# Performance work log

Measured on AMD Instinct MI355X. Metric: run time of the kernel, lower is better.

Reference implementation:

```python
import jax, jax.numpy as jnp
import numpy as np

N, DIN, C, E = 50000, 256, 8, 1600000
N_STEPS = 5


def setup_inputs() -> dict:
    key = jax.random.key(0)
    k1, k2, k3, k4 = jax.random.split(key, 4)
    x = jax.random.normal(k1, (N, DIN), dtype=jnp.float32)
    W = jax.random.normal(k2, (DIN, C), dtype=jnp.float32) / np.float32(np.sqrt(DIN))
    b = jnp.zeros((C,), dtype=jnp.float32)
    edge_index = jax.random.randint(k3, (2, E), 0, N, dtype=jnp.int64)
    rv = jax.random.randint(k4, (E,), 0, E, dtype=jnp.int64)
    return {"x": x, "W": W, "b": b, "edge_index": edge_index, "rv": rv}


def _log_normalize(lx):
    return lx - jax.scipy.special.logsumexp(lx, axis=-1, keepdims=True)


def reference(x, W, b, edge_index, rv):
    # transform: Linear (num_hidden=0) + LogSoftmax -> initial log beliefs
    log_b0 = jax.nn.log_softmax(x @ W + b, axis=-1)            # [N, C]
    src, dst = edge_index[0], edge_index[1]
    n_nodes, n_cls = log_b0.shape
    # learn_coupling=False: log_H = -3 * (ones - eye)
    logH = -3.0 * (jnp.ones((n_cls, n_cls), jnp.float32) - jnp.eye(n_cls, dtype=jnp.float32))
    log_msg = jnp.full((edge_index.shape[1], n_cls), -np.log(n_cls), dtype=jnp.float32)
    log_b = log_b0
    for _ in range(N_STEPS):
        x_j = log_b[src]                                        # [E, C] gather
        t = x_j - log_msg[rv]                                   # [E, C]
        # per-edge logsumexp over incoming class dim against coupling matrix
        raw = jax.scipy.special.logsumexp(t[:, :, None] + logH[None, :, :], axis=1)  # [E, C]
        log_msg = _log_normalize(raw)
        agg = jax.ops.segment_sum(log_msg, dst, num_segments=n_nodes)  # scatter-add
        log_b = _log_normalize(agg + log_b0)
    return log_b
```

## Files before the change

### kernel.cpp

```cpp
#include <hip/hip_runtime.h>

static constexpr int kN   = 50000;
static constexpr int kDin = 256;
static constexpr int kC   = 8;
static constexpr int kE   = 1600000;
static constexpr int kSteps = 5;

static constexpr int kNB      = 256;
static constexpr int kBucketW = 196;
static constexpr int kChunk   = 4096;
static constexpr int kEperB   = kE / kNB;

static constexpr size_t OFF_LOGB0 = 0;
static constexpr size_t OFF_BHIST = 1600000;
static constexpr size_t OFF_GBASE = 1601024;
static constexpr size_t OFF_GCUR  = 1602112;
static constexpr size_t OFF_START = 1603200;
static constexpr size_t OFF_REC   = 1803264;
static constexpr size_t OFF_INV   = 8203264;
static constexpr size_t OFF_MSGA  = 14603264;
static constexpr size_t OFF_MSGB  = 40203264;
static constexpr size_t OFF_SPOS  = 65803264;
static constexpr size_t OFF_SRCS  = 72203264;
static constexpr size_t OFF_RVS   = 78603264;
static constexpr size_t OFF_REC2  = 85003264;
static constexpr size_t OFF_GCUR2 = 97803264;
static constexpr size_t WS_NEEDED = 97804288;

static constexpr float kDEC   = 3.0f / 65535.0f;
static constexpr float kENC   = 65535.0f / 3.0f;
static constexpr float kOFF   = 3.2990003f;
static constexpr float kA     = 0.049787068367863944f;
static constexpr float kOneMA = 0.950212931632136f;

__global__ void __launch_bounds__(256) init_kernel(
    const float* __restrict__ x, const float* __restrict__ W,
    const float* __restrict__ bias,
    float* __restrict__ log_b0, float* __restrict__ log_b,
    const int* __restrict__ dst, int* __restrict__ bhist)
{
    __shared__ int h[kNB];
    if (blockIdx.x >= 1024) {
        h[threadIdx.x] = 0;
        __syncthreads();
        const int nthr = 256 * 256;
        for (int e = (blockIdx.x - 1024) * 256 + threadIdx.x; e < kE; e += nthr)
            atomicAdd(&h[dst[e] / kBucketW], 1);
        __syncthreads();
        if (h[threadIdx.x]) atomicAdd(&bhist[threadIdx.x], h[threadIdx.x]);
        return;
    }

    const int lane   = threadIdx.x & 63;
    const int wave   = (blockIdx.x * 256 + threadIdx.x) >> 6;
    const int nwaves = (1024 * 256) >> 6;

    float w[4][8];
#pragma unroll
    for (int j = 0; j < 4; ++j) {
        const float4* wp = reinterpret_cast<const float4*>(W + (size_t)(lane + 64 * j) * kC);
        float4 a = wp[0], b2 = wp[1];
        w[j][0] = a.x;  w[j][1] = a.y;  w[j][2] = a.z;  w[j][3] = a.w;
        w[j][4] = b2.x; w[j][5] = b2.y; w[j][6] = b2.z; w[j][7] = b2.w;
    }

    for (int row = wave; row < kN; row += nwaves) {
        const float* xr = x + (size_t)row * kDin;
        float acc[8] = {0.f, 0.f, 0.f, 0.f, 0.f, 0.f, 0.f, 0.f};
#pragma unroll
        for (int j = 0; j < 4; ++j) {
            float xv = xr[lane + 64 * j];
#pragma unroll
            for (int c = 0; c < 8; ++c) acc[c] = fmaf(xv, w[j][c], acc[c]);
        }
#pragma unroll
        for (int off = 32; off > 0; off >>= 1) {
#pragma unroll
            for (int c = 0; c < 8; ++c) acc[c] += __shfl_down(acc[c], off, 64);
        }
        if (lane == 0) {
            float z[8], m = -1e30f;
#pragma unroll
            for (int c = 0; c < 8; ++c) { z[c] = acc[c] + bias[c]; m = fmaxf(m, z[c]); }
            float s = 0.f;
#pragma unroll
            for (int c = 0; c < 8; ++c) s += __expf(z[c] - m);
            float lse = m + __logf(s);
#pragma unroll
            for (int c = 0; c < 8; ++c) {
                float v = z[c] - lse;
                log_b0[(size_t)row * 8 + c] = v;
                log_b[(size_t)row * 8 + c]  = v;
            }
        }
    }
}

__global__ void __launch_bounds__(256) bucket_scan_kernel(
    const int* __restrict__ bhist, int* __restrict__ gbase, int* __restrict__ gcur,
    int* __restrict__ gcur2)
{
    __shared__ int sh[kNB];
    const int tid = threadIdx.x;
    int v = bhist[tid];
    sh[tid] = v;
    __syncthreads();
#pragma unroll
    for (int off = 1; off < kNB; off <<= 1) {
        int t = (tid >= off) ? sh[tid - off] : 0;
        __syncthreads();
        sh[tid] += t;
        __syncthreads();
    }
    int excl = sh[tid] - v;
    gbase[tid] = excl;
    gcur[tid]  = excl;
    gcur2[tid] = tid * kEperB;
    if (tid == kNB - 1) { gbase[kNB] = sh[tid]; gcur[kNB] = sh[tid]; }
}

__global__ void __launch_bounds__(256) bin_kernel(
    const int* __restrict__ dst, int* __restrict__ gcur,
    unsigned int* __restrict__ recbuf)
{
    __shared__ int hist[kNB];
    __shared__ int sh[kNB];
    __shared__ int cursor[kNB];
    __shared__ int gdbase[kNB];
    __shared__ unsigned int buf[kChunk];

    const int tid = threadIdx.x;
    const int e0  = blockIdx.x * kChunk;
    const int n   = (kE - e0 < kChunk) ? (kE - e0) : kChunk;

    hist[tid] = 0;
    __syncthreads();

    int myb[16];
    unsigned int rec[16];
#pragma unroll
    for (int k = 0; k < 16; ++k) {
        const int i = tid + k * 256;
        myb[k] = -1;
        if (i < n) {
            const int d = dst[e0 + i];
            const int b = d / kBucketW;
            myb[k] = b;
            rec[k] = ((unsigned int)(d - b * kBucketW) << 21) | (unsigned int)(e0 + i);
            atomicAdd(&hist[b], 1);
        }
    }
    __syncthreads();

    const int cnt = hist[tid];
    sh[tid] = cnt;
    __syncthreads();
#pragma unroll
    for (int off = 1; off < kNB; off <<= 1) {
        int t = (tid >= off) ? sh[tid - off] : 0;
        __syncthreads();
        sh[tid] += t;
        __syncthreads();
    }
    const int excl = sh[tid] - cnt;
    cursor[tid] = excl;
    __syncthreads();

#pragma unroll
    for (int k = 0; k < 16; ++k) {
        if (myb[k] >= 0) {
            int slot = atomicAdd(&cursor[myb[k]], 1);
            buf[slot] = rec[k];
        }
    }
    gdbase[tid] = (cnt > 0) ? atomicAdd(&gcur[tid], cnt) : 0;
    __syncthreads();

    for (int i = tid; i < n; i += 256) {
        int b = 0;
#pragma unroll
        for (int step = 128; step >= 1; step >>= 1)
            if (b + step <= kNB - 1 && sh[b + step - 1] <= i) b += step;
        const int off_in_b = i - (sh[b] - hist[b]);
        recbuf[gdbase[b] + off_in_b] = buf[i];
    }
}

__global__ void __launch_bounds__(256) fine_kernel(
    const int* __restrict__ gbase, const unsigned int* __restrict__ recbuf,
    int* __restrict__ start, int* __restrict__ inv)
{
    __shared__ int hist[kNB];
    __shared__ int sh[kNB];
    __shared__ int lcur[kNB];

    const int tid = threadIdx.x;
    const int b   = blockIdx.x;
    const int nb0 = b * kBucketW;
    const int nnode = (kN - nb0 < kBucketW) ? (kN - nb0) : kBucketW;
    const int rb = gbase[b], re = gbase[b + 1];

    hist[tid] = 0;
    __syncthreads();

    for (int i = rb + tid; i < re; i += 256)
        atomicAdd(&hist[recbuf[i] >> 21], 1);
    __syncthreads();

    const int cnt = hist[tid];
    sh[tid] = cnt;
    __syncthreads();
#pragma unroll
    for (int off = 1; off < kNB; off <<= 1) {
        int t = (tid >= off) ? sh[tid - off] : 0;
        __syncthreads();
        sh[tid] += t;
        __syncthreads();
    }
    const int excl = sh[tid] - cnt;
    lcur[tid] = rb + excl;
    if (tid < nnode) start[nb0 + tid] = rb + excl;
    if (b == gridDim.x - 1 && tid == 0) start[kN] = kE;
    __syncthreads();

    for (int i = rb + tid; i < re; i += 256) {
        const unsigned int r = recbuf[i];
        const int p = atomicAdd(&lcur[r >> 21], 1);
        inv[p] = (int)(r & 0x1FFFFFu);
    }
}

__global__ void __launch_bounds__(256) bin2_kernel(
    const int* __restrict__ inv, int* __restrict__ gcur2,
    unsigned long long* __restrict__ recbuf2)
{
    __shared__ int hist[kNB];
    __shared__ int sh[kNB];
    __shared__ int cursor[kNB];
    __shared__ int gdbase[kNB];
    __shared__ unsigned long long buf[kChunk];

    const int tid = threadIdx.x;
    const int p0  = blockIdx.x * kChunk;
    const int n   = (kE - p0 < kChunk) ? (kE - p0) : kChunk;

    hist[tid] = 0;
    __syncthreads();

    int myb[16];
    unsigned long long rec[16];
#pragma unroll
    for (int k = 0; k < 16; ++k) {
        const int i = tid + k * 256;
        myb[k] = -1;
        if (i < n) {
            const int e = inv[p0 + i];
            const int b = e / kEperB;
            myb[k] = b;
            rec[k] = ((unsigned long long)(e - b * kEperB) << 32) | (unsigned int)(p0 + i);
            atomicAdd(&hist[b], 1);
        }
    }
    __syncthreads();

    const int cnt = hist[tid];
    sh[tid] = cnt;
    __syncthreads();
#pragma unroll
    for (int off = 1; off < kNB; off <<= 1) {
        int t = (tid >= off) ? sh[tid - off] : 0;
        __syncthreads();
        sh[tid] += t;
        __syncthreads();
    }
    const int excl = sh[tid] - cnt;
    cursor[tid] = excl;
    __syncthreads();

#pragma unroll
    for (int k = 0; k < 16; ++k) {
        if (myb[k] >= 0) {
            int slot = atomicAdd(&cursor[myb[k]], 1);
            buf[slot] = rec[k];
        }
    }
    gdbase[tid] = (cnt > 0) ? atomicAdd(&gcur2[tid], cnt) : 0;
    __syncthreads();

    for (int i = tid; i < n; i += 256) {
        int b = 0;
#pragma unroll
        for (int step = 128; step >= 1; step >>= 1)
            if (b + step <= kNB - 1 && sh[b + step - 1] <= i) b += step;
        const int off_in_b = i - (sh[b] - hist[b]);
        recbuf2[gdbase[b] + off_in_b] = buf[i];
    }
}

__global__ void __launch_bounds__(256) fine2_kernel(
    const unsigned long long* __restrict__ recbuf2, int* __restrict__ spos)
{
    __shared__ int slot[kEperB];
    const int tid  = threadIdx.x;
    const int base = blockIdx.x * kEperB;

    for (int i = tid; i < kEperB; i += 256) {
        const unsigned long long r = recbuf2[base + i];
        slot[(int)(r >> 32)] = (int)(r & 0xFFFFFFFFu);
    }
    __syncthreads();
    for (int i = tid; i < kEperB; i += 256)
        spos[base + i] = slot[i];
}

__global__ void __launch_bounds__(256) build_kernel(
    const int* __restrict__ inv, const int* __restrict__ src,
    const int* __restrict__ rv, const int* __restrict__ spos,
    int* __restrict__ src_s, int* __restrict__ rv_s)
{
    const int p0 = (blockIdx.x * 256 + threadIdx.x) * 2;
    if (p0 >= kE) return;
    const int2 ee = *reinterpret_cast<const int2*>(inv + p0);
    const int sx = src[ee.x], sy = src[ee.y];
    const int rx = rv[ee.x],  ry = rv[ee.y];
    const int qx = spos[rx],  qy = spos[ry];
    *reinterpret_cast<int2*>(src_s + p0) = make_int2(sx, sy);
    *reinterpret_cast<int2*>(rv_s + p0)  = make_int2(qx, qy);
}

template <bool FIRST>
__global__ void __launch_bounds__(256) edge_kernel(
    const int* __restrict__ src_s, const int* __restrict__ rv_s,
    const float* __restrict__ log_b,
    const unsigned short* __restrict__ mold,
    unsigned short* __restrict__ mnew)
{
    const int i0 = (blockIdx.x * 256 + threadIdx.x) * 2;
    if (i0 >= kE) return;

    const int2 sp = *reinterpret_cast<const int2*>(src_s + i0);

    const float4* lba = reinterpret_cast<const float4*>(log_b + (size_t)sp.x * 8);
    const float4* lbb = reinterpret_cast<const float4*>(log_b + (size_t)sp.y * 8);
    float4 a0 = lba[0], a1 = lba[1];
    float4 b0 = lbb[0], b1 = lbb[1];

    uint4 ma, mb;
    if (!FIRST) {
        const int2 rp = *reinterpret_cast<const int2*>(rv_s + i0);
        ma = *reinterpret_cast<const uint4*>(mold + (size_t)rp.x * 8);
        mb = *reinterpret_cast<const uint4*>(mold + (size_t)rp.y * 8);
    }

    float ta[8] = {a0.x, a0.y, a0.z, a0.w, a1.x, a1.y, a1.z, a1.w};
    float tb[8] = {b0.x, b0.y, b0.z, b0.w, b1.x, b1.y, b1.z, b1.w};
    if (!FIRST) {
        ta[0] -= (float)(ma.x & 0xffffu) * kDEC;  ta[1] -= (float)(ma.x >> 16) * kDEC;
        ta[2] -= (float)(ma.y & 0xffffu) * kDEC;  ta[3] -= (float)(ma.y >> 16) * kDEC;
        ta[4] -= (float)(ma.z & 0xffffu) * kDEC;  ta[5] -= (float)(ma.z >> 16) * kDEC;
        ta[6] -= (float)(ma.w & 0xffffu) * kDEC;  ta[7] -= (float)(ma.w >> 16) * kDEC;
        tb[0] -= (float)(mb.x & 0xffffu) * kDEC;  tb[1] -= (float)(mb.x >> 16) * kDEC;
        tb[2] -= (float)(mb.y & 0xffffu) * kDEC;  tb[3] -= (float)(mb.y >> 16) * kDEC;
        tb[4] -= (float)(mb.z & 0xffffu) * kDEC;  tb[5] -= (float)(mb.z >> 16) * kDEC;
        tb[6] -= (float)(mb.w & 0xffffu) * kDEC;  tb[7] -= (float)(mb.w >> 16) * kDEC;
    }

    unsigned int qa[8], qb[8];
    {
        float mx = ta[0];
#pragma unroll
        for (int c = 1; c < 8; ++c) mx = fmaxf(mx, ta[c]);
        float p[8], S = 0.f;
#pragma unroll
        for (int c = 0; c < 8; ++c) { p[c] = __expf(ta[c] - mx); S += p[c]; }
        const float coef = kOneMA / S;
#pragma unroll
        for (int c = 0; c < 8; ++c) {
            float u  = fmaf(coef, p[c], kA);
            float qq = fmaf(__logf(u), kENC, 65535.0f);
            qq = fminf(fmaxf(qq + 0.5f, 0.0f), 65535.0f);
            qa[c] = (unsigned int)qq;
        }
    }
    {
        float mx = tb[0];
#pragma unroll
        for (int c = 1; c < 8; ++c) mx = fmaxf(mx, tb[c]);
        float p[8], S = 0.f;
#pragma unroll
        for (int c = 0; c < 8; ++c) { p[c] = __expf(tb[c] - mx); S += p[c]; }
        const float coef = kOneMA / S;
#pragma unroll
        for (int c = 0; c < 8; ++c) {
            float u  = fmaf(coef, p[c], kA);
            float qq = fmaf(__logf(u), kENC, 65535.0f);
            qq = fminf(fmaxf(qq + 0.5f, 0.0f), 65535.0f);
            qb[c] = (unsigned int)qq;
        }
    }

    uint4* mn = reinterpret_cast<uint4*>(mnew + (size_t)i0 * 8);
    mn[0] = make_uint4(qa[0] | (qa[1] << 16), qa[2] | (qa[3] << 16),
                       qa[4] | (qa[5] << 16), qa[6] | (qa[7] << 16));
    mn[1] = make_uint4(qb[0] | (qb[1] << 16), qb[2] | (qb[3] << 16),
                       qb[4] | (qb[5] << 16), qb[6] | (qb[7] << 16));
}

template <bool FINAL>
__global__ void __launch_bounds__(256) node_kernel(
    const int* __restrict__ start,
    const unsigned short* __restrict__ msgq,
    const float* __restrict__ log_b0, float* __restrict__ log_b)
{
    const int wid  = (blockIdx.x * 256 + threadIdx.x) >> 6;
    const int lane = threadIdx.x & 63;
    const int half = lane >> 5;
    const int l32  = lane & 31;
    const int n = wid * 2 + half;
    if (n >= kN) return;

    const int s = start[n], e2 = start[n + 1];

    int q[8] = {0, 0, 0, 0, 0, 0, 0, 0};
    for (int j = s + l32; j < e2; j += 32) {
        const uint4 m = *reinterpret_cast<const uint4*>(msgq + (size_t)j * 8);
        q[0] += (int)(m.x & 0xffffu);  q[1] += (int)(m.x >> 16);
        q[2] += (int)(m.y & 0xffffu);  q[3] += (int)(m.y >> 16);
        q[4] += (int)(m.z & 0xffffu);  q[5] += (int)(m.z >> 16);
        q[6] += (int)(m.w & 0xffffu);  q[7] += (int)(m.w >> 16);
    }
#pragma unroll
    for (int off = 1; off <= 16; off <<= 1) {
#pragma unroll
        for (int c = 0; c < 8; ++c) q[c] += __shfl_xor(q[c], off, 64);
    }

    if (l32 == 0) {
        const int deg = e2 - s;
        const float base = -kOFF * (float)deg;
        const float4* lb0 = reinterpret_cast<const float4*>(log_b0 + (size_t)n * 8);
        float4 c0 = lb0[0], c1 = lb0[1];
        float v[8];
        v[0] = fmaf((float)q[0], kDEC, base) + c0.x;
        v[1] = fmaf((float)q[1], kDEC, base) + c0.y;
        v[2] = fmaf((float)q[2], kDEC, base) + c0.z;
        v[3] = fmaf((float)q[3], kDEC, base) + c0.w;
        v[4] = fmaf((float)q[4], kDEC, base) + c1.x;
        v[5] = fmaf((float)q[5], kDEC, base) + c1.y;
        v[6] = fmaf((float)q[6], kDEC, base) + c1.z;
        v[7] = fmaf((float)q[7], kDEC, base) + c1.w;
        if (FINAL) {
            float m = v[0];
#pragma unroll
            for (int c = 1; c < 8; ++c) m = fmaxf(m, v[c]);
            float sum = 0.f;
#pragma unroll
            for (int c = 0; c < 8; ++c) sum += __expf(v[c] - m);
            float lse = m + __logf(sum);
#pragma unroll
            for (int c = 0; c < 8; ++c) v[c] -= lse;
        }
        float4* lb = reinterpret_cast<float4*>(log_b + (size_t)n * 8);
        lb[0] = make_float4(v[0], v[1], v[2], v[3]);
        lb[1] = make_float4(v[4], v[5], v[6], v[7]);
    }
}

extern "C" void kernel_launch(void* const* d_in, const int* in_sizes, int n_in,
                              void* d_out, int out_size, void* d_ws, size_t ws_size,
                              hipStream_t stream) {
    const float* x    = (const float*)d_in[0];
    const float* W    = (const float*)d_in[1];
    const float* bias = (const float*)d_in[2];
    const int*   ei   = (const int*)d_in[3];
    const int*   rv   = (const int*)d_in[4];
    const int* src = ei;
    const int* dst = ei + kE;
    float* out = (float*)d_out;

    if (ws_size < WS_NEEDED) return;

    char* ws = (char*)d_ws;
    float* log_b0 = (float*)(ws + OFF_LOGB0);
    int*   bhist  = (int*)(ws + OFF_BHIST);
    int*   gbase  = (int*)(ws + OFF_GBASE);
    int*   gcur   = (int*)(ws + OFF_GCUR);
    int*   start  = (int*)(ws + OFF_START);
    unsigned int* recbuf = (unsigned int*)(ws + OFF_REC);
    int*   inv    = (int*)(ws + OFF_INV);
    unsigned short* msgA = (unsigned short*)(ws + OFF_MSGA);
    unsigned short* msgB = (unsigned short*)(ws + OFF_MSGB);
    int*   spos   = (int*)(ws + OFF_SPOS);
    int*   src_s  = (int*)(ws + OFF_SRCS);
    int*   rv_s   = (int*)(ws + OFF_RVS);
    unsigned long long* recbuf2 = (unsigned long long*)(ws + OFF_REC2);
    int*   gcur2  = (int*)(ws + OFF_GCUR2);

    const int edgeBlocks = (kE / 2 + 255) / 256;
    const int nodeBlocks = ((kN + 1) / 2 * 64 + 255) / 256;
    const int binBlocks  = (kE + kChunk - 1) / kChunk;

    (void)hipMemsetAsync(bhist, 0, kNB * sizeof(int), stream);
    init_kernel<<<1280, 256, 0, stream>>>(x, W, bias, log_b0, out, dst, bhist);
    bucket_scan_kernel<<<1, 256, 0, stream>>>(bhist, gbase, gcur, gcur2);
    bin_kernel<<<binBlocks, 256, 0, stream>>>(dst, gcur, recbuf);
    fine_kernel<<<kNB, 256, 0, stream>>>(gbase, recbuf, start, inv);
    bin2_kernel<<<binBlocks, 256, 0, stream>>>(inv, gcur2, recbuf2);
    fine2_kernel<<<kNB, 256, 0, stream>>>(recbuf2, spos);
    build_kernel<<<edgeBlocks, 256, 0, stream>>>(inv, src, rv, spos, src_s, rv_s);

    edge_kernel<true><<<edgeBlocks, 256, 0, stream>>>(src_s, rv_s, out, msgB, msgA);
    node_kernel<false><<<nodeBlocks, 256, 0, stream>>>(start, msgA, log_b0, out);

    unsigned short* cur = msgA;
    unsigned short* nxt = msgB;
    for (int it = 1; it < kSteps; ++it) {
        edge_kernel<false><<<edgeBlocks, 256, 0, stream>>>(src_s, rv_s, out, cur, nxt);
        if (it == kSteps - 1)
            node_kernel<true><<<nodeBlocks, 256, 0, stream>>>(start, nxt, log_b0, out);
        else
            node_kernel<false><<<nodeBlocks, 256, 0, stream>>>(start, nxt, log_b0, out);
        unsigned short* tmp = cur; cur = nxt; nxt = tmp;
    }
}
```

Measured before the change: 505.9 us.

## Carry src/rv payload through sort and store sorted src as 16-bit

Instead of gathering src and rv through the inverse permutation in build_kernel, bin_kernel packs src and rv into a 64-bit payload that travels with the sort records, and fine_kernel writes the sorted src and rv directly. Sorted src indices are stored as unsigned short, which halves index traffic in every edge_kernel launch. This removes random gathers from build_kernel but adds a 64-bit payload buffer and doubles shared memory in bin_kernel (32KB extra LDS), which may reduce occupancy. Packing src into 16 bits relies on N fitting in 16 bits, which holds for N=50000.

```diff
diff --git a/kernel.cpp b/kernel.cpp
--- a/kernel.cpp
+++ b/kernel.cpp
@@ -17,15 +17,17 @@
 static constexpr size_t OFF_GCUR  = 1602112;
 static constexpr size_t OFF_START = 1603200;
 static constexpr size_t OFF_REC   = 1803264;
-static constexpr size_t OFF_INV   = 8203264;
-static constexpr size_t OFF_MSGA  = 14603264;
-static constexpr size_t OFF_MSGB  = 40203264;
-static constexpr size_t OFF_SPOS  = 65803264;
-static constexpr size_t OFF_SRCS  = 72203264;
-static constexpr size_t OFF_RVS   = 78603264;
-static constexpr size_t OFF_REC2  = 85003264;
-static constexpr size_t OFF_GCUR2 = 97803264;
-static constexpr size_t WS_NEEDED = 97804288;
+static constexpr size_t OFF_PAY   = 8203264;
+static constexpr size_t OFF_INV   = 21003264;
+static constexpr size_t OFF_MSGA  = 27403264;
+static constexpr size_t OFF_MSGB  = 53003264;
+static constexpr size_t OFF_SPOS  = 78603264;
+static constexpr size_t OFF_SRCS  = 85003264;
+static constexpr size_t OFF_RVT   = 88203264;
+static constexpr size_t OFF_RVS   = 94603264;
+static constexpr size_t OFF_REC2  = 101003264;
+static constexpr size_t OFF_GCUR2 = 113803264;
+static constexpr size_t WS_NEEDED = 113804288;
 
 static constexpr float kDEC   = 3.0f / 65535.0f;
 static constexpr float kENC   = 65535.0f / 3.0f;
@@ -120,14 +122,16 @@
 }
 
 __global__ void __launch_bounds__(256) bin_kernel(
-    const int* __restrict__ dst, int* __restrict__ gcur,
-    unsigned int* __restrict__ recbuf)
+    const int* __restrict__ dst, const int* __restrict__ src,
+    const int* __restrict__ rv, int* __restrict__ gcur,
+    unsigned int* __restrict__ recbuf, unsigned long long* __restrict__ paybuf)
 {
     __shared__ int hist[kNB];
     __shared__ int sh[kNB];
     __shared__ int cursor[kNB];
     __shared__ int gdbase[kNB];
     __shared__ unsigned int buf[kChunk];
+    __shared__ unsigned long long pbuf[kChunk];
 
     const int tid = threadIdx.x;
     const int e0  = blockIdx.x * kChunk;
@@ -138,6 +142,7 @@
 
     int myb[16];
     unsigned int rec[16];
+    unsigned long long pay[16];
 #pragma unroll
     for (int k = 0; k < 16; ++k) {
         const int i = tid + k * 256;
@@ -147,6 +152,8 @@
             const int b = d / kBucketW;
             myb[k] = b;
             rec[k] = ((unsigned int)(d - b * kBucketW) << 21) | (unsigned int)(e0 + i);
+            pay[k] = ((unsigned long long)(unsigned int)src[e0 + i] << 21)
+                   | (unsigned int)rv[e0 + i];
             atomicAdd(&hist[b], 1);
         }
     }
@@ -170,7 +177,8 @@
     for (int k = 0; k < 16; ++k) {
         if (myb[k] >= 0) {
             int slot = atomicAdd(&cursor[myb[k]], 1);
-            buf[slot] = rec[k];
+            buf[slot]  = rec[k];
+            pbuf[slot] = pay[k];
         }
     }
     gdbase[tid] = (cnt > 0) ? atomicAdd(&gcur[tid], cnt) : 0;
@@ -183,12 +191,15 @@
             if (b + step <= kNB - 1 && sh[b + step - 1] <= i) b += step;
         const int off_in_b = i - (sh[b] - hist[b]);
         recbuf[gdbase[b] + off_in_b] = buf[i];
+        paybuf[gdbase[b] + off_in_b] = pbuf[i];
     }
 }
 
 __global__ void __launch_bounds__(256) fine_kernel(
     const int* __restrict__ gbase, const unsigned int* __restrict__ recbuf,
-    int* __restrict__ start, int* __restrict__ inv)
+    const unsigned long long* __restrict__ paybuf,
+    int* __restrict__ start, int* __restrict__ inv,
+    unsigned short* __restrict__ src_s, int* __restrict__ rvt)
 {
     __shared__ int hist[kNB];
     __shared__ int sh[kNB];
@@ -225,8 +236,11 @@
 
     for (int i = rb + tid; i < re; i += 256) {
         const unsigned int r = recbuf[i];
+        const unsigned long long pay = paybuf[i];
         const int p = atomicAdd(&lcur[r >> 21], 1);
-        inv[p] = (int)(r & 0x1FFFFFu);
+        inv[p]   = (int)(r & 0x1FFFFFu);
+        src_s[p] = (unsigned short)(pay >> 21);
+        rvt[p]   = (int)(pay & 0x1FFFFFu);
     }
 }
 
@@ -314,23 +328,18 @@
 }
 
 __global__ void __launch_bounds__(256) build_kernel(
-    const int* __restrict__ inv, const int* __restrict__ src,
-    const int* __restrict__ rv, const int* __restrict__ spos,
-    int* __restrict__ src_s, int* __restrict__ rv_s)
+    const int* __restrict__ rvt, const int* __restrict__ spos,
+    int* __restrict__ rv_s)
 {
     const int p0 = (blockIdx.x * 256 + threadIdx.x) * 2;
     if (p0 >= kE) return;
-    const int2 ee = *reinterpret_cast<const int2*>(inv + p0);
-    const int sx = src[ee.x], sy = src[ee.y];
-    const int rx = rv[ee.x],  ry = rv[ee.y];
-    const int qx = spos[rx],  qy = spos[ry];
-    *reinterpret_cast<int2*>(src_s + p0) = make_int2(sx, sy);
-    *reinterpret_cast<int2*>(rv_s + p0)  = make_int2(qx, qy);
+    const int2 rr = *reinterpret_cast<const int2*>(rvt + p0);
+    *reinterpret_cast<int2*>(rv_s + p0) = make_int2(spos[rr.x], spos[rr.y]);
 }
 
 template <bool FIRST>
 __global__ void __launch_bounds__(256) edge_kernel(
-    const int* __restrict__ src_s, const int* __restrict__ rv_s,
+    const unsigned short* __restrict__ src_s, const int* __restrict__ rv_s,
     const float* __restrict__ log_b,
     const unsigned short* __restrict__ mold,
     unsigned short* __restrict__ mnew)
@@ -338,7 +347,7 @@
     const int i0 = (blockIdx.x * 256 + threadIdx.x) * 2;
     if (i0 >= kE) return;
 
-    const int2 sp = *reinterpret_cast<const int2*>(src_s + i0);
+    const ushort2 sp = *reinterpret_cast<const ushort2*>(src_s + i0);
 
     const float4* lba = reinterpret_cast<const float4*>(log_b + (size_t)sp.x * 8);
     const float4* lbb = reinterpret_cast<const float4*>(log_b + (size_t)sp.y * 8);
@@ -486,12 +495,14 @@
     int*   gbase  = (int*)(ws + OFF_GBASE);
     int*   gcur   = (int*)(ws + OFF_GCUR);
     int*   start  = (int*)(ws + OFF_START);
-    unsigned int* recbuf = (unsigned int*)(ws + OFF_REC);
+    unsigned int*       recbuf = (unsigned int*)(ws + OFF_REC);
+    unsigned long long* paybuf = (unsigned long long*)(ws + OFF_PAY);
     int*   inv    = (int*)(ws + OFF_INV);
     unsigned short* msgA = (unsigned short*)(ws + OFF_MSGA);
     unsigned short* msgB = (unsigned short*)(ws + OFF_MSGB);
     int*   spos   = (int*)(ws + OFF_SPOS);
-    int*   src_s  = (int*)(ws + OFF_SRCS);
+    unsigned short* src_s = (unsigned short*)(ws + OFF_SRCS);
+    int*   rvt    = (int*)(ws + OFF_RVT);
     int*   rv_s   = (int*)(ws + OFF_RVS);
     unsigned long long* recbuf2 = (unsigned long long*)(ws + OFF_REC2);
     int*   gcur2  = (int*)(ws + OFF_GCUR2);
@@ -503,11 +514,11 @@
     (void)hipMemsetAsync(bhist, 0, kNB * sizeof(int), stream);
     init_kernel<<<1280, 256, 0, stream>>>(x, W, bias, log_b0, out, dst, bhist);
     bucket_scan_kernel<<<1, 256, 0, stream>>>(bhist, gbase, gcur, gcur2);
-    bin_kernel<<<binBlocks, 256, 0, stream>>>(dst, gcur, recbuf);
-    fine_kernel<<<kNB, 256, 0, stream>>>(gbase, recbuf, start, inv);
+    bin_kernel<<<binBlocks, 256, 0, stream>>>(dst, src, rv, gcur, recbuf, paybuf);
+    fine_kernel<<<kNB, 256, 0, stream>>>(gbase, recbuf, paybuf, start, inv, src_s, rvt);
     bin2_kernel<<<binBlocks, 256, 0, stream>>>(inv, gcur2, recbuf2);
     fine2_kernel<<<kNB, 256, 0, stream>>>(recbuf2, spos);
-    build_kernel<<<edgeBlocks, 256, 0, stream>>>(inv, src, rv, spos, src_s, rv_s);
+    build_kernel<<<edgeBlocks, 256, 0, stream>>>(rvt, spos, rv_s);
 
     edge_kernel<true><<<edgeBlocks, 256, 0, stream>>>(src_s, rv_s, out, msgB, msgA);
     node_kernel<false><<<nodeBlocks, 256, 0, stream>>>(start, msgA, log_b0, out);
```

After: 470.7 us. 7.0% less time.
